# Performance work log

Measured on AMD Instinct MI355X. Metric: run time of the kernel, lower is better.

The kernel has to match this reference:

```python
import jax, jax.numpy as jnp
import numpy as np

B = 4096
DETER = 2048
BLOCKS = 8
HIDDEN = 256
SC, SD = 32, 16
STOCH = SC * SD  # 512
ACT = 17
EMBED = 1024
UNIMIX = 0.01
EPS = 1e-4
DPB = DETER // BLOCKS  # 256


def rmsnorm(x, scale):
    rms = jnp.sqrt(jnp.mean(x * x, axis=-1, keepdims=True) + EPS)
    return x / rms * scale


def dense(x, w, b):
    return x @ w + b


def block_linear(x, kernel, bias):
    # kernel: (out_per_block, in_per_block, blocks)
    bs = x.shape[:-1]
    ipb = x.shape[-1] // BLOCKS
    xg = x.reshape(*bs, BLOCKS, ipb)
    y = jnp.einsum('...gi,oig->...go', xg, kernel)
    return y.reshape(*bs, -1) + bias


def sample(logits):
    # unimix + straight-through argmax
    probs = jax.nn.softmax(logits, axis=-1)
    probs = (1.0 - UNIMIX) * probs + UNIMIX / SD
    logits = jnp.log(probs + 1e-8)
    soft = jax.nn.softmax(logits, axis=-1)
    hard = jax.nn.one_hot(jnp.argmax(logits, axis=-1), SD, dtype=soft.dtype)
    return hard + soft - jax.lax.stop_gradient(soft)


def setup_inputs() -> dict:
    key = jax.random.key(0)
    ks = jax.random.split(key, 16)

    def lecun(k, shape, fan_in):
        return jax.random.normal(k, shape, jnp.float32) / np.sqrt(fan_in)

    return {
        'stoch': jax.random.uniform(ks[0], (B, SC, SD), jnp.float32),
        'deter': jax.random.normal(ks[1], (B, DETER), jnp.float32),
        'action': jax.random.normal(ks[2], (B, ACT), jnp.float32),
        'embed': jax.random.normal(ks[3], (B, EMBED), jnp.float32),
        # Deter net params
        'in0_w': lecun(ks[4], (DETER, HIDDEN), DETER), 'in0_b': jnp.zeros((HIDDEN,)), 'in_norm0_s': jnp.ones((HIDDEN,)),
        'in1_w': lecun(ks[5], (STOCH, HIDDEN), STOCH), 'in1_b': jnp.zeros((HIDDEN,)), 'in_norm1_s': jnp.ones((HIDDEN,)),
        'in2_w': lecun(ks[6], (ACT, HIDDEN), ACT), 'in2_b': jnp.zeros((HIDDEN,)), 'in_norm2_s': jnp.ones((HIDDEN,)),
        'hid0_k': lecun(ks[7], (DPB, DPB + 3 * HIDDEN, BLOCKS), DPB + 3 * HIDDEN),
        'hid0_b': jnp.zeros((DETER,)), 'hid_norm0_s': jnp.ones((DETER,)),
        'gru_k': lecun(ks[8], (3 * DPB, DPB, BLOCKS), DPB), 'gru_b': jnp.zeros((3 * DETER,)),
        # posterior head
        'obs_fc0_w': lecun(ks[9], (DETER + EMBED, HIDDEN), DETER + EMBED), 'obs_fc0_b': jnp.zeros((HIDDEN,)),
        'obs_norm0_s': jnp.ones((HIDDEN,)),
        'obs_out_w': lecun(ks[10], (HIDDEN, STOCH), HIDDEN), 'obs_out_b': jnp.zeros((STOCH,)),
    }


def reference(stoch, deter, action, embed,
              in0_w, in0_b, in_norm0_s, in1_w, in1_b, in_norm1_s,
              in2_w, in2_b, in_norm2_s, hid0_k, hid0_b, hid_norm0_s,
              gru_k, gru_b, obs_fc0_w, obs_fc0_b, obs_norm0_s,
              obs_out_w, obs_out_b):
    Bn = stoch.shape[0]
    stoch_flat = stoch.reshape(Bn, -1)  # (B, 512)
    act = action / jnp.maximum(jnp.abs(action), 1.0)
    x0 = jax.nn.silu(rmsnorm(dense(deter, in0_w, in0_b), in_norm0_s))
    x1 = jax.nn.silu(rmsnorm(dense(stoch_flat, in1_w, in1_b), in_norm1_s))
    x2 = jax.nn.silu(rmsnorm(dense(act, in2_w, in2_b), in_norm2_s))
    x = jnp.concatenate([x0, x1, x2], axis=-1)  # (B, 768)
    x = jnp.broadcast_to(x[:, None, :], (Bn, BLOCKS, x.shape[-1]))
    deter_blocked = deter.reshape(Bn, BLOCKS, DPB)
    x = jnp.concatenate([deter_blocked, x], axis=-1).reshape(Bn, -1)  # (B, 8192)
    x = jax.nn.silu(rmsnorm(block_linear(x, hid0_k, hid0_b), hid_norm0_s))  # (B, 2048)
    gates = block_linear(x, gru_k, gru_b)  # (B, 6144)
    gates = gates.reshape(Bn, BLOCKS, 3 * DPB)
    g0, g1, g2 = jnp.split(gates, 3, axis=-1)
    reset = jax.nn.sigmoid(g0.reshape(Bn, -1))
    cand = g1.reshape(Bn, -1)
    update = jax.nn.sigmoid(g2.reshape(Bn, -1) - 1.0)
    new_deter = update * jnp.tanh(reset * cand) + (1.0 - update) * deter
    # posterior head
    h = jnp.concatenate([new_deter, embed], axis=-1)
    h = jax.nn.silu(rmsnorm(dense(h, obs_fc0_w, obs_fc0_b), obs_norm0_s))
    logit = dense(h, obs_out_w, obs_out_b).reshape(Bn, SC, SD)
    new_stoch = sample(logit)
    return (new_stoch, new_deter, logit)
```

## Files before the change

kernel.cpp:

```cpp
#include <hip/hip_runtime.h>
#include <cmath>

constexpr int BATCH = 4096;
constexpr float EPSN = 1e-4f;

constexpr int OFF_STOCH = 0;
constexpr int OFF_DETER = BATCH * 512;
constexpr int OFF_LOGIT = OFF_DETER + BATCH * 2048;

typedef unsigned short ushort;
typedef __attribute__((ext_vector_type(4))) float f32x4;
typedef __attribute__((ext_vector_type(8))) short s16x8;
struct us4 { ushort x, y, z, w; };

constexpr size_t U_WHH = 0;
constexpr size_t U_WHL = U_WHH + 2097152;
constexpr size_t U_WGH = U_WHL + 2097152;
constexpr size_t U_WGL = U_WGH + 1572864;
constexpr size_t U_WFH = U_WGL + 1572864;
constexpr size_t U_WFL = U_WFH + 786432;
constexpr size_t U_WOH = U_WFL + 786432;
constexpr size_t U_WOL = U_WOH + 131072;
constexpr size_t U_PEND = U_WOL + 131072;
constexpr size_t F_XB = U_PEND / 2;
constexpr size_t F_XH = F_XB + 3145728;
constexpr size_t U_X0H = (F_XH + 6291456) * 2;
constexpr size_t U_X0L = U_X0H + 524288;
constexpr size_t U_X1H = U_X0L + 524288;
constexpr size_t U_X1L = U_X1H + 131072;
constexpr size_t F_HB = F_XH + 4194304;

#define DINLINE __device__ __forceinline__

DINLINE float sigm(float x)  { return 1.0f / (1.0f + expf(-x)); }
DINLINE float siluf(float x) { return x / (1.0f + expf(-x)); }

DINLINE float4 ld4(const float* p) { return *reinterpret_cast<const float4*>(p); }
DINLINE void st4(float* p, float4 v) { *reinterpret_cast<float4*>(p) = v; }

DINLINE ushort f2bf(float x) {
  unsigned u = __float_as_uint(x);
  unsigned r = u + 0x7fffu + ((u >> 16) & 1u);
  return (ushort)(r >> 16);
}
DINLINE float bf2f(ushort h) { return __uint_as_float(((unsigned)h) << 16); }

DINLINE void cp16g(void* lds, const void* g) {
  __builtin_amdgcn_global_load_lds(
      (const __attribute__((address_space(1))) unsigned int*)g,
      (__attribute__((address_space(3))) unsigned int*)lds, 16, 0, 0);
}

DINLINE f32x4 mfma16(s16x8 a, s16x8 b, f32x4 c) {
  return __builtin_amdgcn_mfma_f32_16x16x32_bf16(a, b, c, 0, 0, 0);
}

DINLINE int swz_addr(int row, int kb0) {
  return (row * 64 + kb0) ^ ((row & 7) << 4);
}
DINLINE void dec_swz(int D, int& row, int& kb) {
  int r2 = (D >> 8) & 1;
  int r0 = ((D >> 6) & 1) ^ r2;
  row = ((D >> 7) << 1) | r0;
  kb = (D & 48) ^ ((row & 3) << 4);
}

DINLINE void split2(float x, ushort& h, ushort& l) {
  h = f2bf(x);
  l = f2bf(x - bf2f(h));
}

DINLINE size_t frag_idx(int n, int k, int NK) {
  return ((size_t)((n >> 4) * NK + (k >> 5)) * 64 + ((k >> 3) & 3) * 16 + (n & 15)) * 8 + (k & 7);
}

DINLINE float4 rms_silu4(float v0, float v1, float v2, float v3, float4 s4) {
  float ss = v0 * v0 + v1 * v1 + v2 * v2 + v3 * v3;
#pragma unroll
  for (int off = 32; off; off >>= 1) ss += __shfl_xor(ss, off);
  float inv = 1.0f / sqrtf(ss * (1.0f / 256.0f) + EPSN);
  float4 o;
  o.x = siluf(v0 * inv * s4.x); o.y = siluf(v1 * inv * s4.y);
  o.z = siluf(v2 * inv * s4.z); o.w = siluf(v3 * inv * s4.w);
  return o;
}

__global__ __launch_bounds__(256) void k_prep(
    const float* __restrict__ hk, const float* __restrict__ gk,
    const float* __restrict__ w0, const float* __restrict__ w1,
    const float* __restrict__ wf, const float* __restrict__ wo,
    ushort* __restrict__ wsU) {
  __shared__ float L[64 * 65];
  const int bid = blockIdx.x, tid = threadIdx.x;
  if (bid < 1792) {
    int t = bid * 256 + tid;
    if (t < 262144) {
      int o = t >> 10, i = t & 1023;
      const float* src = hk + (size_t)t * 8;
      float4 v0 = ld4(src), v1 = ld4(src + 4);
      float vv[8] = {v0.x, v0.y, v0.z, v0.w, v1.x, v1.y, v1.z, v1.w};
      size_t fi = frag_idx(o, i, 32);
#pragma unroll
      for (int g2 = 0; g2 < 8; ++g2) {
        ushort h, l; split2(vv[g2], h, l);
        wsU[U_WHH + (size_t)g2 * 262144 + fi] = h;
        wsU[U_WHL + (size_t)g2 * 262144 + fi] = l;
      }
    } else {
      int e = t - 262144;
      int o = e >> 8, i = e & 255;
      const float* src = gk + (size_t)e * 8;
      float4 v0 = ld4(src), v1 = ld4(src + 4);
      float vv[8] = {v0.x, v0.y, v0.z, v0.w, v1.x, v1.y, v1.z, v1.w};
      int gate = o >> 8, nc = (o >> 6) & 3, srow = gate * 64 + (o & 63);
      size_t fi = frag_idx(srow, i, 8);
#pragma unroll
      for (int g2 = 0; g2 < 8; ++g2) {
        ushort h, l; split2(vv[g2], h, l);
        size_t pb = (size_t)(g2 * 4 + nc) * 49152;
        wsU[U_WGH + pb + fi] = h;
        wsU[U_WGL + pb + fi] = l;
      }
    }
    return;
  }
  int t = bid - 1792;
  const float* src; ushort* dh; ushort* dl; int K, N;
  if (t < 128)      { src = w0; dh = wsU + U_X0H; dl = wsU + U_X0L; K = 2048; N = 256; }
  else if (t < 160) { t -= 128; src = w1; dh = wsU + U_X1H; dl = wsU + U_X1L; K = 512;  N = 256; }
  else if (t < 352) { t -= 160; src = wf; dh = wsU + U_WFH; dl = wsU + U_WFL; K = 3072; N = 256; }
  else              { t -= 352; src = wo; dh = wsU + U_WOH; dl = wsU + U_WOL; K = 256;  N = 512; }
  const int NK = K / 32;
  const int ntiles = N / 64;
  const int k0 = (t / ntiles) * 64, n0 = (t % ntiles) * 64;
#pragma unroll
  for (int q = 0; q < 4; ++q) {
    int row = q * 16 + (tid >> 4), col = (tid & 15) * 4;
    float4 v = ld4(src + (size_t)(k0 + row) * N + n0 + col);
    L[row * 65 + col]     = v.x;
    L[row * 65 + col + 1] = v.y;
    L[row * 65 + col + 2] = v.z;
    L[row * 65 + col + 3] = v.w;
  }
  __syncthreads();
  const int nl = tid >> 2, kc = (tid & 3) * 16;
  const int ng = n0 + nl;
  s16x8 h0, h1, l0v, l1v;
#pragma unroll
  for (int j = 0; j < 16; ++j) {
    ushort h, l; split2(L[(kc + j) * 65 + nl], h, l);
    if (j < 8) { h0[j] = (short)h; l0v[j] = (short)l; }
    else       { h1[j - 8] = (short)h; l1v[j - 8] = (short)l; }
  }
  size_t fa = frag_idx(ng, k0 + kc, NK);
  size_t fb = frag_idx(ng, k0 + kc + 8, NK);
  *(s16x8*)(dh + fa) = h0;
  *(s16x8*)(dh + fb) = h1;
  *(s16x8*)(dl + fa) = l0v;
  *(s16x8*)(dl + fb) = l1v;
}

__global__ __launch_bounds__(512) void k_gemm256(
    int mode,
    const float* __restrict__ deter, const float* __restrict__ stoch,
    const float* __restrict__ newdet, const float* __restrict__ embed,
    const ushort* __restrict__ wsU, float* __restrict__ part) {
  __shared__ ushort Ah[2][64 * 32], Al[2][64 * 32];
  const int tid = threadIdx.x, lane = tid & 63, wv = tid >> 6;
  const int wr = wv >> 2, wc = wv & 3;
  const int bid = blockIdx.x;
  constexpr size_t PL0 = (size_t)4096 * 512;

  const float* A0; const float* A1 = nullptr;
  int lda0, lda1 = 0, ksw = 1 << 30;
  const ushort* wFh; const ushort* wFl;
  int NKt, kch0, kbase, KT, m0, dstride, dcol;
  float* dst;

  if (mode == 0) {
    if (bid < 256) {
      int ks = bid & 3; m0 = (bid >> 2) * 64; kbase = ks * 512; KT = 16;
      A0 = deter; lda0 = 2048;
      wFh = wsU + U_X0H; wFl = wsU + U_X0L; NKt = 64; kch0 = ks * 16;
      dst = part + (size_t)(ks >> 1) * PL0; dstride = 512; dcol = (ks & 1) * 256;
    } else {
      int b = bid - 256; int ks = b & 1; m0 = (b >> 1) * 64; kbase = ks * 256; KT = 8;
      A0 = stoch; lda0 = 512;
      wFh = wsU + U_X1H; wFl = wsU + U_X1L; NKt = 16; kch0 = ks * 8;
      dst = part + 2 * PL0; dstride = 512; dcol = ks * 256;
    }
  } else {
    int ks = bid & 3; m0 = (bid >> 2) * 64; kbase = ks * 768; KT = 24;
    A0 = newdet; lda0 = 2048; A1 = embed; lda1 = 1024; ksw = 2048;
    wFh = wsU + U_WFH; wFl = wsU + U_WFL; NKt = 96; kch0 = ks * 24;
    dst = part + (size_t)ks * 4096 * 256; dstride = 256; dcol = 0;
  }

  const int arow = tid >> 2, akq = (tid & 3) * 8;
  const int abyte = swz_addr(arow, (tid & 3) * 16);
  float av[8];
  s16x8 bh[4], bl[4];

  const f32x4 z4 = {0.f, 0.f, 0.f, 0.f};
  f32x4 acc[2][4];
#pragma unroll
  for (int i = 0; i < 2; ++i)
#pragma unroll
    for (int j = 0; j < 4; ++j) acc[i][j] = z4;

#define U_LOADA(kt) \
  if (tid < 256) { \
    int kg = kbase + (kt) * 32 + akq; \
    const float* p = (kg < ksw) ? A0 + (size_t)(m0 + arow) * lda0 + kg \
                                : A1 + (size_t)(m0 + arow) * lda1 + (kg - ksw); \
    float4 u_ = ld4(p), w_ = ld4(p + 4); \
    av[0] = u_.x; av[1] = u_.y; av[2] = u_.z; av[3] = u_.w; \
    av[4] = w_.x; av[5] = w_.y; av[6] = w_.z; av[7] = w_.w; \
  }
#define U_WRITEA(buf) \
  if (tid < 256) { \
    s16x8 h8, l8; \
    _Pragma("unroll") \
    for (int j = 0; j < 8; ++j) { \
      ushort h_, l_; split2(av[j], h_, l_); \
      h8[j] = (short)h_; l8[j] = (short)l_; \
    } \
    *(s16x8*)((char*)Ah[buf] + abyte) = h8; \
    *(s16x8*)((char*)Al[buf] + abyte) = l8; \
  }
#define U_LOADB(kt) { \
    _Pragma("unroll") \
    for (int nf = 0; nf < 4; ++nf) { \
      size_t fo = ((size_t)((wc * 4 + nf) * NKt + kch0 + (kt)) * 64 + lane) * 8; \
      bh[nf] = *(const s16x8*)(wFh + fo); \
      bl[nf] = *(const s16x8*)(wFl + fo); \
    } }

  U_LOADA(0);
  U_WRITEA(0);
  U_LOADB(0);
  __syncthreads();
  int cur = 0;
  for (int t = 0; t < KT; ++t) {
    if (t + 1 < KT) { U_LOADA(t + 1); }
    const int k16 = (lane >> 4) * 16;
    s16x8 afh[2], afl[2];
#pragma unroll
    for (int mf = 0; mf < 2; ++mf) {
      int by = swz_addr(wr * 32 + mf * 16 + (lane & 15), k16);
      afh[mf] = *(const s16x8*)((const char*)Ah[cur] + by);
      afl[mf] = *(const s16x8*)((const char*)Al[cur] + by);
    }
#pragma unroll
    for (int nf = 0; nf < 4; ++nf) {
#pragma unroll
      for (int mf = 0; mf < 2; ++mf) {
        acc[mf][nf] = mfma16(afh[mf], bh[nf], acc[mf][nf]);
        acc[mf][nf] = mfma16(afh[mf], bl[nf], acc[mf][nf]);
        acc[mf][nf] = mfma16(afl[mf], bh[nf], acc[mf][nf]);
      }
    }
    if (t + 1 < KT) { U_LOADB(t + 1); U_WRITEA(cur ^ 1); }
    __syncthreads();
    cur ^= 1;
  }
#undef U_LOADA
#undef U_WRITEA
#undef U_LOADB
#pragma unroll
  for (int mf = 0; mf < 2; ++mf) {
    int rbase = m0 + wr * 32 + mf * 16 + ((lane >> 4) << 2);
#pragma unroll
    for (int nf = 0; nf < 4; ++nf) {
      int col = dcol + wc * 64 + nf * 16 + (lane & 15);
#pragma unroll
      for (int r = 0; r < 4; ++r)
        dst[(size_t)(rbase + r) * dstride + col] = acc[mf][nf][r];
    }
  }
}

__global__ __launch_bounds__(256) void k_x2(
    const float* __restrict__ action, const float* __restrict__ w2,
    const float* __restrict__ b2, const float* __restrict__ s2,
    ushort* __restrict__ xbp) {
  __shared__ float W2s[17 * 256];
  __shared__ float A2s[16 * 20];
  const int tid = threadIdx.x, tx = tid & 63, wv = tid >> 6;
  const int m0 = blockIdx.x * 16;
  for (int e = tid; e < 17 * 256; e += 256) W2s[e] = w2[e];
  for (int e = tid; e < 272; e += 256) {
    int r = e / 17, c = e % 17;
    float a = action[(size_t)(m0 + r) * 17 + c];
    float m = fabsf(a);
    A2s[r * 20 + c] = a / (m > 1.f ? m : 1.f);
  }
  __syncthreads();
  float4 acc2[4];
#pragma unroll
  for (int r = 0; r < 4; ++r) acc2[r] = make_float4(0.f, 0.f, 0.f, 0.f);
#pragma unroll
  for (int k = 0; k < 17; ++k) {
    float4 w4 = ld4(W2s + k * 256 + tx * 4);
#pragma unroll
    for (int r = 0; r < 4; ++r) {
      float av = A2s[(wv * 4 + r) * 20 + k];
      acc2[r].x = fmaf(av, w4.x, acc2[r].x);
      acc2[r].y = fmaf(av, w4.y, acc2[r].y);
      acc2[r].z = fmaf(av, w4.z, acc2[r].z);
      acc2[r].w = fmaf(av, w4.w, acc2[r].w);
    }
  }
  float4 b4 = ld4(b2 + tx * 4);
  float4 s4 = ld4(s2 + tx * 4);
#pragma unroll
  for (int r = 0; r < 4; ++r) {
    float4 o = rms_silu4(acc2[r].x + b4.x, acc2[r].y + b4.y,
                         acc2[r].z + b4.z, acc2[r].w + b4.w, s4);
    us4 h4, l4;
    split2(o.x, h4.x, l4.x); split2(o.y, h4.y, l4.y);
    split2(o.z, h4.z, l4.z); split2(o.w, h4.w, l4.w);
    size_t rb = (size_t)(m0 + wv * 4 + r) * 1536;
    *(us4*)(xbp + rb + 512 + tx * 4) = h4;
    *(us4*)(xbp + rb + 768 + 512 + tx * 4) = l4;
  }
}

__global__ __launch_bounds__(256) void k_comb_in(
    const float* __restrict__ part,
    const float* __restrict__ b0, const float* __restrict__ s0,
    const float* __restrict__ b1, const float* __restrict__ s1,
    ushort* __restrict__ xbp) {
  const int tid = threadIdx.x, tx = tid & 63, wv = tid >> 6;
  const size_t row = blockIdx.x * 2 + (wv >> 1);
  const int half = wv & 1;
  constexpr size_t PL = (size_t)4096 * 512;
  float4 v = make_float4(0.f, 0.f, 0.f, 0.f);
  if (half == 0) {
#pragma unroll
    for (int p = 0; p < 2; ++p) {
      const float* s = part + p * PL + row * 512 + tx * 4;
      float4 a = ld4(s), b = ld4(s + 256);
      v.x += a.x + b.x; v.y += a.y + b.y; v.z += a.z + b.z; v.w += a.w + b.w;
    }
  } else {
    const float* s = part + 2 * PL + row * 512 + tx * 4;
    float4 a = ld4(s), b = ld4(s + 256);
    v.x = a.x + b.x; v.y = a.y + b.y; v.z = a.z + b.z; v.w = a.w + b.w;
  }
  const float* bp = half ? b1 : b0;
  const float* sp = half ? s1 : s0;
  float4 b4 = ld4(bp + tx * 4);
  float4 s4 = ld4(sp + tx * 4);
  float4 o = rms_silu4(v.x + b4.x, v.y + b4.y, v.z + b4.z, v.w + b4.w, s4);
  us4 h4, l4;
  split2(o.x, h4.x, l4.x); split2(o.y, h4.y, l4.y);
  split2(o.z, h4.z, l4.z); split2(o.w, h4.w, l4.w);
  *(us4*)(xbp + row * 1536 + half * 256 + tx * 4) = h4;
  *(us4*)(xbp + row * 1536 + 768 + half * 256 + tx * 4) = l4;
}

__global__ __launch_bounds__(256) void k_comb4(
    const float* __restrict__ part, const float* __restrict__ bias,
    const float* __restrict__ scale, ushort* __restrict__ hbp) {
  const int tid = threadIdx.x, tx = tid & 63, wv = tid >> 6;
  const size_t row = blockIdx.x * 4 + wv;
  float4 v = make_float4(0.f, 0.f, 0.f, 0.f);
#pragma unroll
  for (int ks = 0; ks < 4; ++ks) {
    float4 t = ld4(part + (size_t)ks * 4096 * 256 + row * 256 + tx * 4);
    v.x += t.x; v.y += t.y; v.z += t.z; v.w += t.w;
  }
  float4 b4 = ld4(bias + tx * 4);
  float4 s4 = ld4(scale + tx * 4);
  float4 o = rms_silu4(v.x + b4.x, v.y + b4.y, v.z + b4.z, v.w + b4.w, s4);
  us4 h4, l4;
  split2(o.x, h4.x, l4.x); split2(o.y, h4.y, l4.y);
  split2(o.z, h4.z, l4.z); split2(o.w, h4.w, l4.w);
  *(us4*)(hbp + row * 512 + tx * 4) = h4;
  *(us4*)(hbp + row * 512 + 256 + tx * 4) = l4;
}

__global__ __launch_bounds__(512) void k_hid0m(
    const float* __restrict__ deter, const ushort* __restrict__ xbp,
    const ushort* __restrict__ wsU,
    const float* __restrict__ hbias, float* __restrict__ yh) {
  __shared__ ushort Ah[2][64 * 32], Al[2][64 * 32];
  const int tid = threadIdx.x, lane = tid & 63, wv = tid >> 6;
  const int wr = wv >> 2, wc = wv & 3;
  const int g = blockIdx.x & 7;
  const int m0 = (int)(blockIdx.x >> 3) * 64;

  const ushort* whFh = wsU + U_WHH + (size_t)g * 262144;
  const ushort* whFl = wsU + U_WHL + (size_t)g * 262144;
  const char* xbB = (const char*)xbp;

  const int arow = tid >> 2, akq = (tid & 3) * 8;
  const int abyte = swz_addr(arow, (tid & 3) * 16);
  int an0, akb;
  dec_swz(tid * 16, an0, akb);
  float av[8];
  s16x8 bh[4], bl[4];

  const f32x4 z4 = {0.f, 0.f, 0.f, 0.f};
  f32x4 acc[2][4];
#pragma unroll
  for (int i = 0; i < 2; ++i)
#pragma unroll
    for (int j = 0; j < 4; ++j) acc[i][j] = z4;

#define H_LOADA_DET(kt) \
  if (tid < 256) { \
    const float* p = deter + (size_t)(m0 + arow) * 2048 + g * 256 + (kt) * 32 + akq; \
    float4 u_ = ld4(p), w_ = ld4(p + 4); \
    av[0] = u_.x; av[1] = u_.y; av[2] = u_.z; av[3] = u_.w; \
    av[4] = w_.x; av[5] = w_.y; av[6] = w_.z; av[7] = w_.w; \
  }
#define H_WRITEA(buf) \
  if (tid < 256) { \
    s16x8 h8, l8; \
    _Pragma("unroll") \
    for (int j = 0; j < 8; ++j) { \
      ushort h_, l_; split2(av[j], h_, l_); \
      h8[j] = (short)h_; l8[j] = (short)l_; \
    } \
    *(s16x8*)((char*)Ah[buf] + abyte) = h8; \
    *(s16x8*)((char*)Al[buf] + abyte) = l8; \
  }
#define H_ISSUEA(buf, kt) \
  if (tid < 256) { \
    size_t rb = (size_t)(m0 + an0) * 3072; \
    int co = ((kt) * 32 - 256) * 2 + akb; \
    cp16g((char*)Ah[buf] + tid * 16, xbB + rb + co); \
    cp16g((char*)Al[buf] + tid * 16, xbB + rb + 1536 + co); \
  }
#define H_LOADB(kt) { \
    _Pragma("unroll") \
    for (int nf = 0; nf < 4; ++nf) { \
      size_t fo = ((size_t)((wc * 4 + nf) * 32 + (kt)) * 64 + lane) * 8; \
      bh[nf] = *(const s16x8*)(whFh + fo); \
      bl[nf] = *(const s16x8*)(whFl + fo); \
    } }

  H_LOADA_DET(0);
  H_WRITEA(0);
  H_LOADB(0);
  __syncthreads();
  int cur = 0;
  for (int t = 0; t < 32; ++t) {
    const bool pf = (t + 1 < 32);
    const bool det = (t + 1 < 8);
    if (pf) {
      if (det) { H_LOADA_DET(t + 1); }
      else     { H_ISSUEA(cur ^ 1, t + 1); }
    }
    const int k16 = (lane >> 4) * 16;
    s16x8 afh[2], afl[2];
#pragma unroll
    for (int mf = 0; mf < 2; ++mf) {
      int by = swz_addr(wr * 32 + mf * 16 + (lane & 15), k16);
      afh[mf] = *(const s16x8*)((const char*)Ah[cur] + by);
      afl[mf] = *(const s16x8*)((const char*)Al[cur] + by);
    }
#pragma unroll
    for (int nf = 0; nf < 4; ++nf) {
#pragma unroll
      for (int mf = 0; mf < 2; ++mf) {
        acc[mf][nf] = mfma16(afh[mf], bh[nf], acc[mf][nf]);
        acc[mf][nf] = mfma16(afh[mf], bl[nf], acc[mf][nf]);
        acc[mf][nf] = mfma16(afl[mf], bh[nf], acc[mf][nf]);
      }
    }
    if (pf) { H_LOADB(t + 1); }
    if (pf && det) { H_WRITEA(cur ^ 1); }
    __syncthreads();
    cur ^= 1;
  }
#undef H_LOADA_DET
#undef H_WRITEA
#undef H_ISSUEA
#undef H_LOADB
#pragma unroll
  for (int mf = 0; mf < 2; ++mf) {
    int rbase = m0 + wr * 32 + mf * 16 + ((lane >> 4) << 2);
#pragma unroll
    for (int nf = 0; nf < 4; ++nf) {
      int col = wc * 64 + nf * 16 + (lane & 15);
      float b = hbias[g * 256 + col];
#pragma unroll
      for (int r = 0; r < 4; ++r)
        yh[(size_t)(rbase + r) * 2048 + g * 256 + col] = acc[mf][nf][r] + b;
    }
  }
}

__global__ __launch_bounds__(256) void k_rmsnorm2048(
    float* __restrict__ xh, const float* __restrict__ scale) {
  const int b = blockIdx.x, tid = threadIdx.x;
  float* row = xh + (size_t)b * 2048;
  float4 v0 = ld4(row + tid * 8);
  float4 v1 = ld4(row + tid * 8 + 4);
  float ss = v0.x * v0.x + v0.y * v0.y + v0.z * v0.z + v0.w * v0.w +
             v1.x * v1.x + v1.y * v1.y + v1.z * v1.z + v1.w * v1.w;
#pragma unroll
  for (int off = 32; off; off >>= 1) ss += __shfl_xor(ss, off);
  __shared__ float wsum[4];
  if ((tid & 63) == 0) wsum[tid >> 6] = ss;
  __syncthreads();
  float tot = wsum[0] + wsum[1] + wsum[2] + wsum[3];
  float inv = 1.0f / sqrtf(tot * (1.0f / 2048.0f) + EPSN);
  float4 sc0 = ld4(scale + tid * 8);
  float4 sc1 = ld4(scale + tid * 8 + 4);
  float o[8];
  o[0] = siluf(v0.x * inv * sc0.x); o[1] = siluf(v0.y * inv * sc0.y);
  o[2] = siluf(v0.z * inv * sc0.z); o[3] = siluf(v0.w * inv * sc0.w);
  o[4] = siluf(v1.x * inv * sc1.x); o[5] = siluf(v1.y * inv * sc1.y);
  o[6] = siluf(v1.z * inv * sc1.z); o[7] = siluf(v1.w * inv * sc1.w);
  s16x8 h8, l8;
#pragma unroll
  for (int j = 0; j < 8; ++j) {
    ushort h, l; split2(o[j], h, l);
    h8[j] = (short)h; l8[j] = (short)l;
  }
  ushort* rp = (ushort*)row;
  *(s16x8*)(rp + tid * 8) = h8;
  *(s16x8*)(rp + 2048 + tid * 8) = l8;
}

__global__ __launch_bounds__(512) void k_grum(
    const ushort* __restrict__ xhp, const ushort* __restrict__ wsU,
    const float* __restrict__ gb, const float* __restrict__ deter,
    float* __restrict__ newdet) {
  __shared__ ushort Ah[8][64 * 32], Al[8][64 * 32];
  const int tid = threadIdx.x, lane = tid & 63, wv = tid >> 6;
  const int wr = wv >> 2, wc = wv & 3;
  const int g = blockIdx.x & 7;
  const int nc = (int)(blockIdx.x >> 3) & 3;
  const int m0 = (int)(blockIdx.x >> 5) * 64;

  const ushort* wgFh = wsU + U_WGH + (size_t)(g * 4 + nc) * 49152;
  const ushort* wgFl = wsU + U_WGL + (size_t)(g * 4 + nc) * 49152;
  const char* xhB = (const char*)xhp;

#pragma unroll
  for (int q = 0; q < 4; ++q) {
    int lin = q * 8192 + tid * 16;
    int chunk = lin >> 12;
    int within = lin & 4095;
    int row, kb;
    dec_swz(within, row, kb);
    size_t src = (size_t)(m0 + row) * 8192 + (size_t)(g * 256 + chunk * 32) * 2 + kb;
    cp16g((char*)Ah + lin, xhB + src);
    cp16g((char*)Al + lin, xhB + src + 4096);
  }
  __syncthreads();

  const f32x4 z4 = {0.f, 0.f, 0.f, 0.f};
  f32x4 acc[2][3];
#pragma unroll
  for (int i = 0; i < 2; ++i)
#pragma unroll
    for (int j = 0; j < 3; ++j) acc[i][j] = z4;

#pragma unroll
  for (int t = 0; t < 8; ++t) {
    s16x8 bh[3], bl[3];
#pragma unroll
    for (int gt = 0; gt < 3; ++gt) {
      size_t fo = ((size_t)((gt * 4 + wc) * 8 + t) * 64 + lane) * 8;
      bh[gt] = *(const s16x8*)(wgFh + fo);
      bl[gt] = *(const s16x8*)(wgFl + fo);
    }
    const int k16 = (lane >> 4) * 16;
    s16x8 afh[2], afl[2];
#pragma unroll
    for (int mf = 0; mf < 2; ++mf) {
      int by = swz_addr(wr * 32 + mf * 16 + (lane & 15), k16);
      afh[mf] = *(const s16x8*)((const char*)Ah[t] + by);
      afl[mf] = *(const s16x8*)((const char*)Al[t] + by);
    }
#pragma unroll
    for (int gt = 0; gt < 3; ++gt) {
#pragma unroll
      for (int mf = 0; mf < 2; ++mf) {
        acc[mf][gt] = mfma16(afh[mf], bh[gt], acc[mf][gt]);
        acc[mf][gt] = mfma16(afh[mf], bl[gt], acc[mf][gt]);
        acc[mf][gt] = mfma16(afl[mf], bh[gt], acc[mf][gt]);
      }
    }
  }
  const int col = nc * 64 + wc * 16 + (lane & 15);
  const float br = gb[g * 768 + col];
  const float bc = gb[g * 768 + 256 + col];
  const float bu = gb[g * 768 + 512 + col];
#pragma unroll
  for (int mf = 0; mf < 2; ++mf) {
    int rbase = m0 + wr * 32 + mf * 16 + ((lane >> 4) << 2);
#pragma unroll
    for (int r = 0; r < 4; ++r) {
      int row = rbase + r;
      float rr = sigm(acc[mf][0][r] + br);
      float cc = acc[mf][1][r] + bc;
      float uu = sigm(acc[mf][2][r] + bu - 1.0f);
      float d = deter[(size_t)row * 2048 + g * 256 + col];
      newdet[(size_t)row * 2048 + g * 256 + col] =
          uu * tanhf(rr * cc) + (1.0f - uu) * d;
    }
  }
}

__global__ __launch_bounds__(512) void k_obsoutm(
    const ushort* __restrict__ hbp, const ushort* __restrict__ wsU,
    const float* __restrict__ ob, float* __restrict__ logit) {
  __shared__ ushort Ah[2][64 * 32], Al[2][64 * 32];
  const int tid = threadIdx.x, lane = tid & 63, wv = tid >> 6;
  const int wr = wv >> 2, wc = wv & 3;
  const int half = blockIdx.x & 1;
  const int m0 = (int)(blockIdx.x >> 1) * 64;

  const ushort* woFh = wsU + U_WOH;
  const ushort* woFl = wsU + U_WOL;
  const char* hbB = (const char*)hbp;
  int an0, akb;
  dec_swz(tid * 16, an0, akb);
  s16x8 bh[4], bl[4];

  const f32x4 z4 = {0.f, 0.f, 0.f, 0.f};
  f32x4 acc[2][4];
#pragma unroll
  for (int i = 0; i < 2; ++i)
#pragma unroll
    for (int j = 0; j < 4; ++j) acc[i][j] = z4;

#define O_ISSUEA(buf, kt) \
  if (tid < 256) { \
    size_t rb = (size_t)(m0 + an0) * 1024; \
    int co = (kt) * 64 + akb; \
    cp16g((char*)Ah[buf] + tid * 16, hbB + rb + co); \
    cp16g((char*)Al[buf] + tid * 16, hbB + rb + 512 + co); \
  }
#define O_LOADB(kt) { \
    _Pragma("unroll") \
    for (int nf = 0; nf < 4; ++nf) { \
      size_t fo = ((size_t)((half * 16 + wc * 4 + nf) * 8 + (kt)) * 64 + lane) * 8; \
      bh[nf] = *(const s16x8*)(woFh + fo); \
      bl[nf] = *(const s16x8*)(woFl + fo); \
    } }

  O_ISSUEA(0, 0);
  O_LOADB(0);
  __syncthreads();
  int cur = 0;
  for (int t = 0; t < 8; ++t) {
    if (t + 1 < 8) { O_ISSUEA(cur ^ 1, t + 1); }
    const int k16 = (lane >> 4) * 16;
    s16x8 afh[2], afl[2];
#pragma unroll
    for (int mf = 0; mf < 2; ++mf) {
      int by = swz_addr(wr * 32 + mf * 16 + (lane & 15), k16);
      afh[mf] = *(const s16x8*)((const char*)Ah[cur] + by);
      afl[mf] = *(const s16x8*)((const char*)Al[cur] + by);
    }
#pragma unroll
    for (int nf = 0; nf < 4; ++nf) {
#pragma unroll
      for (int mf = 0; mf < 2; ++mf) {
        acc[mf][nf] = mfma16(afh[mf], bh[nf], acc[mf][nf]);
        acc[mf][nf] = mfma16(afh[mf], bl[nf], acc[mf][nf]);
        acc[mf][nf] = mfma16(afl[mf], bh[nf], acc[mf][nf]);
      }
    }
    if (t + 1 < 8) { O_LOADB(t + 1); }
    __syncthreads();
    cur ^= 1;
  }
#undef O_ISSUEA
#undef O_LOADB
#pragma unroll
  for (int mf = 0; mf < 2; ++mf) {
    int rbase = m0 + wr * 32 + mf * 16 + ((lane >> 4) << 2);
#pragma unroll
    for (int nf = 0; nf < 4; ++nf) {
      int col = half * 256 + wc * 64 + nf * 16 + (lane & 15);
      float b = ob[col];
#pragma unroll
      for (int r = 0; r < 4; ++r)
        logit[(size_t)(rbase + r) * 512 + col] = acc[mf][nf][r] + b;
    }
  }
}

__global__ __launch_bounds__(256) void k_argmax(
    const float* __restrict__ logit, float* __restrict__ stoch_out) {
  const size_t row = blockIdx.x * 4 + (threadIdx.x >> 6);
  const int lane = threadIdx.x & 63;
  const float* lp = logit + row * 512 + lane * 8;
  float4 a = ld4(lp), b = ld4(lp + 4);
  float v[8] = {a.x, a.y, a.z, a.w, b.x, b.y, b.z, b.w};
  float bv = v[0]; int bi = 0;
#pragma unroll
  for (int j = 1; j < 8; ++j)
    if (v[j] > bv) { bv = v[j]; bi = j; }
  bi += lane * 8;
  float pv = __shfl_xor(bv, 1);
  int   pi = __shfl_xor(bi, 1);
  if (pv > bv || (pv == bv && pi < bi)) { bv = pv; bi = pi; }
  float4 o0, o1;
  int base = lane * 8;
  o0.x = (bi == base + 0) ? 1.f : 0.f;
  o0.y = (bi == base + 1) ? 1.f : 0.f;
  o0.z = (bi == base + 2) ? 1.f : 0.f;
  o0.w = (bi == base + 3) ? 1.f : 0.f;
  o1.x = (bi == base + 4) ? 1.f : 0.f;
  o1.y = (bi == base + 5) ? 1.f : 0.f;
  o1.z = (bi == base + 6) ? 1.f : 0.f;
  o1.w = (bi == base + 7) ? 1.f : 0.f;
  st4(stoch_out + row * 512 + base, o0);
  st4(stoch_out + row * 512 + base + 4, o1);
}

extern "C" void kernel_launch(void* const* d_in, const int* in_sizes, int n_in,
                              void* d_out, int out_size, void* d_ws, size_t ws_size,
                              hipStream_t stream) {
  (void)in_sizes; (void)n_in; (void)out_size; (void)ws_size;
  const float* stoch      = (const float*)d_in[0];
  const float* deter      = (const float*)d_in[1];
  const float* action     = (const float*)d_in[2];
  const float* embed      = (const float*)d_in[3];
  const float* in0_w      = (const float*)d_in[4];
  const float* in0_b      = (const float*)d_in[5];
  const float* n0_s       = (const float*)d_in[6];
  const float* in1_w      = (const float*)d_in[7];
  const float* in1_b      = (const float*)d_in[8];
  const float* n1_s       = (const float*)d_in[9];
  const float* in2_w      = (const float*)d_in[10];
  const float* in2_b      = (const float*)d_in[11];
  const float* n2_s       = (const float*)d_in[12];
  const float* hid0_k     = (const float*)d_in[13];
  const float* hid0_b     = (const float*)d_in[14];
  const float* hidn_s     = (const float*)d_in[15];
  const float* gru_k      = (const float*)d_in[16];
  const float* gru_b      = (const float*)d_in[17];
  const float* obs_fc0_w  = (const float*)d_in[18];
  const float* obs_fc0_b  = (const float*)d_in[19];
  const float* obs_n_s    = (const float*)d_in[20];
  const float* obs_out_w  = (const float*)d_in[21];
  const float* obs_out_b  = (const float*)d_in[22];

  float*  out = (float*)d_out;
  float*  ws  = (float*)d_ws;
  ushort* wsU = (ushort*)d_ws;
  ushort* xbp = (ushort*)(ws + F_XB);
  float*  xh  = ws + F_XH;
  ushort* xhp = (ushort*)(ws + F_XH);
  ushort* hbp = (ushort*)(ws + F_HB);
  float*  part = xh;

  hipLaunchKernelGGL(k_prep, dim3(2176), dim3(256), 0, stream,
                     hid0_k, gru_k, in0_w, in1_w, obs_fc0_w, obs_out_w, wsU);
  hipLaunchKernelGGL(k_x2, dim3(256), dim3(256), 0, stream,
                     action, in2_w, in2_b, n2_s, xbp);
  hipLaunchKernelGGL(k_gemm256, dim3(384), dim3(512), 0, stream,
                     0, deter, stoch, out + OFF_DETER, embed, wsU, part);
  hipLaunchKernelGGL(k_comb_in, dim3(2048), dim3(256), 0, stream,
                     part, in0_b, n0_s, in1_b, n1_s, xbp);
  hipLaunchKernelGGL(k_hid0m, dim3(512), dim3(512), 0, stream,
                     deter, xbp, wsU, hid0_b, xh);
  hipLaunchKernelGGL(k_rmsnorm2048, dim3(4096), dim3(256), 0, stream, xh, hidn_s);
  hipLaunchKernelGGL(k_grum, dim3(2048), dim3(512), 0, stream,
                     xhp, wsU, gru_b, deter, out + OFF_DETER);
  hipLaunchKernelGGL(k_gemm256, dim3(256), dim3(512), 0, stream,
                     1, deter, stoch, out + OFF_DETER, embed, wsU, part);
  hipLaunchKernelGGL(k_comb4, dim3(1024), dim3(256), 0, stream,
                     part, obs_fc0_b, obs_n_s, hbp);
  hipLaunchKernelGGL(k_obsoutm, dim3(128), dim3(512), 0, stream,
                     hbp, wsU, obs_out_b, out + OFF_LOGIT);
  hipLaunchKernelGGL(k_argmax, dim3(1024), dim3(256), 0, stream,
                     out + OFF_LOGIT, out + OFF_STOCH);
}
```

Baseline: 215.4 us.

## Compute two GRU column chunks per block to reuse staged activations

Each GRU-gate block now computes two 64-column chunks instead of one, so the activation tile staged into shared memory is reused twice and the grid halves. Weight fragments are software-prefetched one step ahead, with the next chunk's loads issued while the current MFMAs run. This halves redundant activation loads from global memory, at the cost of doubled accumulator registers and fewer blocks for latency hiding.

Result: no change. 217.6 us (+1.0%).

```diff
diff --git a/kernel.cpp b/kernel.cpp
--- a/kernel.cpp
+++ b/kernel.cpp
@@ -535,12 +535,20 @@
   const int tid = threadIdx.x, lane = tid & 63, wv = tid >> 6;
   const int wr = wv >> 2, wc = wv & 3;
   const int g = blockIdx.x & 7;
-  const int nc = (int)(blockIdx.x >> 3) & 3;
-  const int m0 = (int)(blockIdx.x >> 5) * 64;
-
-  const ushort* wgFh = wsU + U_WGH + (size_t)(g * 4 + nc) * 49152;
-  const ushort* wgFl = wsU + U_WGL + (size_t)(g * 4 + nc) * 49152;
+  const int ncp = (int)(blockIdx.x >> 3) & 1;
+  const int m0 = (int)(blockIdx.x >> 4) * 64;
+
+  const ushort* wgFh0 = wsU + U_WGH + (size_t)(g * 4 + ncp * 2) * 49152;
+  const ushort* wgFl0 = wsU + U_WGL + (size_t)(g * 4 + ncp * 2) * 49152;
   const char* xhB = (const char*)xhp;
+
+#define G_LOADBJ(dh_, dl_, j, kt) { \
+    _Pragma("unroll") \
+    for (int gt = 0; gt < 3; ++gt) { \
+      size_t fo = ((size_t)((gt * 4 + wc) * 8 + (kt)) * 64 + lane) * 8 + (size_t)(j) * 49152; \
+      dh_[gt] = *(const s16x8*)(wgFh0 + fo); \
+      dl_[gt] = *(const s16x8*)(wgFl0 + fo); \
+    } }
 
 #pragma unroll
   for (int q = 0; q < 4; ++q) {
@@ -553,24 +561,19 @@
     cp16g((char*)Ah + lin, xhB + src);
     cp16g((char*)Al + lin, xhB + src + 4096);
   }
+  s16x8 bh[3], bl[3];
+  G_LOADBJ(bh, bl, 0, 0);
   __syncthreads();
 
   const f32x4 z4 = {0.f, 0.f, 0.f, 0.f};
-  f32x4 acc[2][3];
+  f32x4 acc0[2][3], acc1[2][3];
 #pragma unroll
   for (int i = 0; i < 2; ++i)
 #pragma unroll
-    for (int j = 0; j < 3; ++j) acc[i][j] = z4;
+    for (int j = 0; j < 3; ++j) { acc0[i][j] = z4; acc1[i][j] = z4; }
 
 #pragma unroll
   for (int t = 0; t < 8; ++t) {
-    s16x8 bh[3], bl[3];
-#pragma unroll
-    for (int gt = 0; gt < 3; ++gt) {
-      size_t fo = ((size_t)((gt * 4 + wc) * 8 + t) * 64 + lane) * 8;
-      bh[gt] = *(const s16x8*)(wgFh + fo);
-      bl[gt] = *(const s16x8*)(wgFl + fo);
-    }
     const int k16 = (lane >> 4) * 16;
     s16x8 afh[2], afl[2];
 #pragma unroll
@@ -583,28 +586,47 @@
     for (int gt = 0; gt < 3; ++gt) {
 #pragma unroll
       for (int mf = 0; mf < 2; ++mf) {
-        acc[mf][gt] = mfma16(afh[mf], bh[gt], acc[mf][gt]);
-        acc[mf][gt] = mfma16(afh[mf], bl[gt], acc[mf][gt]);
-        acc[mf][gt] = mfma16(afl[mf], bh[gt], acc[mf][gt]);
+        acc0[mf][gt] = mfma16(afh[mf], bh[gt], acc0[mf][gt]);
+        acc0[mf][gt] = mfma16(afh[mf], bl[gt], acc0[mf][gt]);
+        acc0[mf][gt] = mfma16(afl[mf], bh[gt], acc0[mf][gt]);
       }
     }
-  }
-  const int col = nc * 64 + wc * 16 + (lane & 15);
-  const float br = gb[g * 768 + col];
-  const float bc = gb[g * 768 + 256 + col];
-  const float bu = gb[g * 768 + 512 + col];
-#pragma unroll
-  for (int mf = 0; mf < 2; ++mf) {
-    int rbase = m0 + wr * 32 + mf * 16 + ((lane >> 4) << 2);
-#pragma unroll
-    for (int r = 0; r < 4; ++r) {
-      int row = rbase + r;
-      float rr = sigm(acc[mf][0][r] + br);
-      float cc = acc[mf][1][r] + bc;
-      float uu = sigm(acc[mf][2][r] + bu - 1.0f);
-      float d = deter[(size_t)row * 2048 + g * 256 + col];
-      newdet[(size_t)row * 2048 + g * 256 + col] =
-          uu * tanhf(rr * cc) + (1.0f - uu) * d;
+    G_LOADBJ(bh, bl, 1, t);
+#pragma unroll
+    for (int gt = 0; gt < 3; ++gt) {
+#pragma unroll
+      for (int mf = 0; mf < 2; ++mf) {
+        acc1[mf][gt] = mfma16(afh[mf], bh[gt], acc1[mf][gt]);
+        acc1[mf][gt] = mfma16(afh[mf], bl[gt], acc1[mf][gt]);
+        acc1[mf][gt] = mfma16(afl[mf], bh[gt], acc1[mf][gt]);
+      }
+    }
+    if (t + 1 < 8) { G_LOADBJ(bh, bl, 0, t + 1); }
+  }
+#undef G_LOADBJ
+
+#pragma unroll
+  for (int j = 0; j < 2; ++j) {
+    const int col = (ncp * 2 + j) * 64 + wc * 16 + (lane & 15);
+    const float br = gb[g * 768 + col];
+    const float bc = gb[g * 768 + 256 + col];
+    const float bu = gb[g * 768 + 512 + col];
+#pragma unroll
+    for (int mf = 0; mf < 2; ++mf) {
+      int rbase = m0 + wr * 32 + mf * 16 + ((lane >> 4) << 2);
+#pragma unroll
+      for (int r = 0; r < 4; ++r) {
+        int row = rbase + r;
+        float a0 = j == 0 ? acc0[mf][0][r] : acc1[mf][0][r];
+        float a1 = j == 0 ? acc0[mf][1][r] : acc1[mf][1][r];
+        float a2 = j == 0 ? acc0[mf][2][r] : acc1[mf][2][r];
+        float rr = sigm(a0 + br);
+        float cc = a1 + bc;
+        float uu = sigm(a2 + bu - 1.0f);
+        float d = deter[(size_t)row * 2048 + g * 256 + col];
+        newdet[(size_t)row * 2048 + g * 256 + col] =
+            uu * tanhf(rr * cc) + (1.0f - uu) * d;
+      }
     }
   }
 }
@@ -767,7 +789,7 @@
   hipLaunchKernelGGL(k_hid0m, dim3(512), dim3(512), 0, stream,
                      deter, xbp, wsU, hid0_b, xh);
   hipLaunchKernelGGL(k_rmsnorm2048, dim3(4096), dim3(256), 0, stream, xh, hidn_s);
-  hipLaunchKernelGGL(k_grum, dim3(2048), dim3(512), 0, stream,
+  hipLaunchKernelGGL(k_grum, dim3(1024), dim3(512), 0, stream,
                      xhp, wsU, gru_b, deter, out + OFF_DETER);
   hipLaunchKernelGGL(k_gemm256, dim3(256), dim3(512), 0, stream,
                      1, deter, stoch, out + OFF_DETER, embed, wsU, part);
```
